# Kernel tuning notes

Measured on AMD Instinct MI355X. Metric: run time of the kernel, lower is better.

Reference implementation:

```python
import jax, jax.numpy as jnp
import numpy as np

NUM_ROUTING = 3

def squash(v, axis=-1):
    # scale = s2 / (1 + s2) / sqrt(s2), same as the TF source (no epsilon)
    s2 = jnp.sum(jnp.square(v), axis=axis, keepdims=True)
    scale = s2 / (1.0 + s2) / jnp.sqrt(s2)
    return scale * v


def setup_inputs() -> dict:
    key = jax.random.key(0)
    k1, k2 = jax.random.split(key)
    B, I, D = 128, 1152, 8   # batch, input_num_capsule, input_dim_vector
    C, E = 32, 16            # num_capsule, dim_vector
    x = jax.random.normal(k1, (B, I, D), dtype=jnp.float32)
    W = jax.random.normal(k2, (I, C, D, E), dtype=jnp.float32) * 0.05
    return {"x": x, "W": W}


def reference(x, W):
    # x: [B, I, D]; W: [I, C, D, E]
    B, I, D = x.shape
    C, E = W.shape[1], W.shape[3]
    # inputs_hat: u_hat[b,i,c,e] = sum_d x[b,i,d] * W[i,c,d,e]
    # (the TF code serializes this over batch via tf.scan; math is a batched GEMM)
    u_hat = jnp.einsum('bid,icde->bice', x, W)  # [B, I, C, E]
    # routing logits; TF bias has shape [1, I, C, 1, 1] and becomes per-batch
    # [B, I, C, 1, 1] after the first += (broadcast). We track [*, I, C].
    b = jnp.zeros((1, I, C), dtype=x.dtype)
    outputs = None
    for i in range(NUM_ROUTING):
        c = jax.nn.softmax(b, axis=2)[..., None]           # [*, I, C, 1]
        s = jnp.sum(c * u_hat, axis=1, keepdims=True)      # [B, 1, C, E]
        outputs = squash(s)                                # [B, 1, C, E]
        if i != NUM_ROUTING - 1:
            b = b + jnp.sum(u_hat * outputs, axis=-1)      # [B, I, C]
    return outputs.reshape(B, C, E)
```

## Files before the change

### kernel.cpp

```cpp
#include <hip/hip_runtime.h>
#include <hip/hip_fp16.h>
#include <math.h>

#define BATCH 128
#define NI    1152
#define ND    8
#define NC    32
#define NE    16
#define NROUT 3

#define ISPLIT     64
#define GTILES     9
#define BT         16
#define NB         4
#define RT_THREADS 256
#define CROW       68
#define TLDSW      (NC * CROW)
#define SQ_THREADS 256
#define PREP_TPB   2

typedef _Float16 h2 __attribute__((ext_vector_type(2)));
typedef unsigned int uint;

__device__ __forceinline__ h2 cvt_pk(float a, float b) {
    auto r = __builtin_amdgcn_cvt_pkrtz(a, b);
    union { decltype(r) i; h2 o; } u; u.i = r; return u.o;
}
__device__ __forceinline__ uint h2u(h2 v) { union { h2 h; uint u; } x; x.h = v; return x.u; }
__device__ __forceinline__ h2 u2h(uint v) { union { uint u; h2 h; } x; x.u = v; return x.h; }

#if __has_builtin(__builtin_amdgcn_fdot2)
#define FDOT2(a, b, c) __builtin_amdgcn_fdot2((a), (b), (c), false)
#else
__device__ __forceinline__ float FDOT2(h2 a, h2 b, float c) {
    return c + (float)a.x * (float)b.x + (float)a.y * (float)b.y;
}
#endif

template<int CTRL>
__device__ __forceinline__ float dpp_add(float v) {
    int t = __builtin_amdgcn_update_dpp(0, __float_as_int(v), CTRL, 0xF, 0xF, true);
    return v + __int_as_float(t);
}

__device__ __forceinline__ float xor32_sum(float v) {
#if __has_builtin(__builtin_amdgcn_permlane32_swap)
    auto r = __builtin_amdgcn_permlane32_swap(__float_as_int(v), __float_as_int(v), false, false);
    return __int_as_float(r[0]) + __int_as_float(r[1]);
#else
    return v + __shfl_xor(v, 32);
#endif
}
__device__ __forceinline__ float xor16_sum(float v) {
#if __has_builtin(__builtin_amdgcn_permlane16_swap)
    auto r = __builtin_amdgcn_permlane16_swap(__float_as_int(v), __float_as_int(v), false, false);
    return __int_as_float(r[0]) + __int_as_float(r[1]);
#else
    int s = __builtin_amdgcn_ds_swizzle(__float_as_int(v), 0x401F);
    return v + __int_as_float(s);
#endif
}

__device__ __forceinline__ float sum_over_e8(float v) {
    v = dpp_add<0xB1>(v);
    v = dpp_add<0x4E>(v);
    v = dpp_add<0x141>(v);
    return v;
}

__global__ __launch_bounds__(RT_THREADS)
void prep_kernel(const float* __restrict__ W, uint* __restrict__ W_hp)
{
    __shared__ float ls[PREP_TPB][NC * 132];

    const int tid = threadIdx.x;
    const size_t i0 = (size_t)blockIdx.x * PREP_TPB;

    const float4* src = (const float4*)(W + i0 * (NC * ND * NE));
#pragma unroll
    for (int t = 0; t < PREP_TPB; ++t) {
#pragma unroll
        for (int r = 0; r < 4; ++r) {
            int g = tid + r * RT_THREADS;
            float4 v = src[t * 1024 + g];
            *(float4*)&ls[t][(g >> 5) * 132 + (g & 31) * 4] = v;
        }
    }
    __syncthreads();

#pragma unroll
    for (int t = 0; t < PREP_TPB; ++t) {
#pragma unroll
        for (int r = 0; r < 2; ++r) {
            int g = tid + r * RT_THREADS;
            int c = g >> 4, e = g & 15;
            const float* p = &ls[t][c * 132 + e];
            uint4 o;
            o.x = h2u(cvt_pk(p[0],  p[16]));
            o.y = h2u(cvt_pk(p[32], p[48]));
            o.z = h2u(cvt_pk(p[64], p[80]));
            o.w = h2u(cvt_pk(p[96], p[112]));
            *(uint4*)&W_hp[(i0 + t) * TLDSW + c * CROW + e * 4] = o;
        }
    }
}

__global__ __launch_bounds__(RT_THREADS)
void route_iter_kernel(const float* __restrict__ x, const uint* __restrict__ W_hp,
                       const float* __restrict__ o_sum, __half* __restrict__ s_part,
                       int iter)
{
    constexpr int ICHUNK_T = NI / ISPLIT;
    constexpr int NGROUP_T = ICHUNK_T / GTILES;
    static_assert(NGROUP_T * GTILES == ICHUNK_T, "group split");

    __shared__ uint Wh[GTILES * TLDSW];

    const int tid = threadIdx.x;
    const int c   = tid & 31;
    const int eh  = (tid >> 5) & 1;
    int wid;
    asm("v_mov_b32 %0, %1" : "=v"(wid) : "v"(tid >> 6));
    const int ic  = blockIdx.x;
    const int bt  = blockIdx.y;
    const int i0  = ic * ICHUNK_T;
    const int b0  = bt * BT + wid * NB;
    const int e0  = eh * 8;

    float o_reg[NB][8];
    if (iter > 0) {
#pragma unroll
        for (int j = 0; j < NB; ++j) {
            const float4* op = (const float4*)(o_sum + ((size_t)(b0 + j) * NC + c) * NE + e0);
            float4 a = op[0], b = op[1];
            o_reg[j][0] = a.x; o_reg[j][1] = a.y; o_reg[j][2] = a.z; o_reg[j][3] = a.w;
            o_reg[j][4] = b.x; o_reg[j][5] = b.y; o_reg[j][6] = b.z; o_reg[j][7] = b.w;
        }
    }

    float s_acc[NB][8];
#pragma unroll
    for (int j = 0; j < NB; ++j)
#pragma unroll
        for (int e = 0; e < 8; ++e) s_acc[j][e] = 0.f;

    const float* xp[NB];
    float4 xnA[NB][2], xnB[NB][2];
#pragma unroll
    for (int j = 0; j < NB; ++j) {
        xp[j] = x + ((size_t)(b0 + j) * NI + i0) * ND;
        xnA[j][0] = *(const float4*)xp[j];
        xnA[j][1] = *(const float4*)(xp[j] + 4);
    }

    const uint* wbase = &Wh[c * CROW + e0 * 4];

    auto body = [&](const float4 (&XC)[NB][2], float4 (&XN)[NB][2], int t, int II) {
        if (II + 1 < ICHUNK_T) {
#pragma unroll
            for (int j = 0; j < NB; ++j) {
                xp[j] += ND;
                XN[j][0] = *(const float4*)xp[j];
                XN[j][1] = *(const float4*)(xp[j] + 4);
            }
        }

        h2 xq[NB][4];
#pragma unroll
        for (int j = 0; j < NB; ++j) {
            xq[j][0] = cvt_pk(XC[j][0].x, XC[j][0].y);
            xq[j][1] = cvt_pk(XC[j][0].z, XC[j][0].w);
            xq[j][2] = cvt_pk(XC[j][1].x, XC[j][1].y);
            xq[j][3] = cvt_pk(XC[j][1].z, XC[j][1].w);
        }

        const uint* wr = wbase + t * TLDSW;
        float uh[NB][8];
#pragma unroll
        for (int er = 0; er < 8; ++er) {
            uint4 wv = *(const uint4*)(wr + er * 4);
            h2 w0 = u2h(wv.x), w1 = u2h(wv.y), w2 = u2h(wv.z), w3 = u2h(wv.w);
#pragma unroll
            for (int j = 0; j < NB; ++j) {
                float acc = 0.f;
                acc = FDOT2(xq[j][0], w0, acc);
                acc = FDOT2(xq[j][1], w1, acc);
                acc = FDOT2(xq[j][2], w2, acc);
                acc = FDOT2(xq[j][3], w3, acc);
                uh[j][er] = acc;
            }
        }

        if (iter > 0) {
#pragma unroll
            for (int j = 0; j < NB; ++j) {
                float lp = 0.f;
#pragma unroll
                for (int e = 0; e < 8; ++e) lp = fmaf(uh[j][e], o_reg[j][e], lp);
                lp = xor32_sum(lp);
                float el = __expf(lp);
                float v = dpp_add<0x140>(dpp_add<0x141>(
                          dpp_add<0x4E>(dpp_add<0xB1>(el))));
                float den = xor16_sum(v);
                float wgt = el * __builtin_amdgcn_rcpf(den);
#pragma unroll
                for (int e = 0; e < 8; ++e) s_acc[j][e] = fmaf(wgt, uh[j][e], s_acc[j][e]);
            }
        } else {
            const float wgt = 1.f / 32.f;
#pragma unroll
            for (int j = 0; j < NB; ++j)
#pragma unroll
                for (int e = 0; e < 8; ++e) s_acc[j][e] = fmaf(wgt, uh[j][e], s_acc[j][e]);
        }
    };

#pragma unroll
    for (int g = 0; g < NGROUP_T; ++g) {
        if (g) __syncthreads();
        {
            constexpr int TOT4 = GTILES * TLDSW / 4;
            const uint4* src = (const uint4*)(W_hp + (size_t)(i0 + g * GTILES) * TLDSW);
            uint4* dst = (uint4*)Wh;
#pragma unroll
            for (int k = 0; k < (TOT4 + RT_THREADS - 1) / RT_THREADS; ++k) {
                int idx = tid + k * RT_THREADS;
                if (TOT4 % RT_THREADS == 0 || idx < TOT4)
                    dst[idx] = src[idx];
            }
        }
        __syncthreads();

#pragma unroll
        for (int tp = 0; tp < GTILES; ++tp) {
            int II = g * GTILES + tp;
            if ((II & 1) == 0) body(xnA, xnB, tp, II);
            else               body(xnB, xnA, tp, II);
        }
    }

#pragma unroll
    for (int j = 0; j < NB; ++j) {
        __half* base = s_part + (((size_t)ic * BATCH + (b0 + j)) * NC + c) * NE + e0;
        union { __half2 h2v[4]; uint4 u; } pk;
#pragma unroll
        for (int q = 0; q < 4; ++q)
            pk.h2v[q] = __floats2half2_rn(s_acc[j][2*q], s_acc[j][2*q+1]);
        *(uint4*)base = pk.u;
    }
}

__global__ __launch_bounds__(SQ_THREADS)
void squash_kernel(const __half* __restrict__ s_part, float* __restrict__ o_sum,
                   float* __restrict__ out, int iter)
{
    const int base2 = (blockIdx.x * SQ_THREADS + threadIdx.x) * 2;

    float a0 = 0.f, a1 = 0.f;
#pragma unroll 8
    for (int k = 0; k < ISPLIT; ++k) {
        __half2 v = *(const __half2*)(s_part + (size_t)k * (BATCH * NC * NE) + base2);
        a0 += __low2float(v);
        a1 += __high2float(v);
    }

    float q = sum_over_e8(a0 * a0 + a1 * a1);
    float scale = sqrtf(q) / (1.f + q);
    float o0 = scale * a0, o1 = scale * a1;

    if (iter == NROUT - 1) {
        *(float2*)(out + base2) = make_float2(o0, o1);
    } else if (iter == 0) {
        *(float2*)(o_sum + base2) = make_float2(o0, o1);
    } else {
        float2 prev = *(float2*)(o_sum + base2);
        *(float2*)(o_sum + base2) = make_float2(prev.x + o0, prev.y + o1);
    }
}

extern "C" void kernel_launch(void* const* d_in, const int* in_sizes, int n_in,
                              void* d_out, int out_size, void* d_ws, size_t ws_size,
                              hipStream_t stream) {
    const float* x = (const float*)d_in[0];
    const float* W = (const float*)d_in[1];
    float* out = (float*)d_out;

    const size_t whp_words = (size_t)NI * TLDSW;
    const size_t slice_h   = (size_t)BATCH * NC * NE;

    uint*   W_hp   = (uint*)d_ws;
    __half* s_part = (__half*)(W_hp + whp_words);
    float*  o_sum  = (float*)(s_part + (size_t)ISPLIT * slice_h);

    prep_kernel<<<NI / PREP_TPB, RT_THREADS, 0, stream>>>(W, W_hp);

    for (int it = 0; it < NROUT; ++it) {
        route_iter_kernel<<<dim3(ISPLIT, BATCH / BT), RT_THREADS, 0, stream>>>(
            x, W_hp, o_sum, s_part, it);
        squash_kernel<<<(BATCH * NC * NE) / (SQ_THREADS * 2), SQ_THREADS, 0, stream>>>(
            s_part, o_sum, out, it);
    }
}
```

Measured before the change: 106.2 us.

## Fuse routing iterations and squash into one persistent kernel with grid barriers

```diff
diff --git a/kernel.cpp b/kernel.cpp
--- a/kernel.cpp
+++ b/kernel.cpp
@@ -10,14 +10,15 @@
 #define NROUT 3
 
 #define ISPLIT     64
-#define GTILES     9
-#define BT         16
+#define ICHUNK     18
+#define BT         32
 #define NB         4
-#define RT_THREADS 256
+#define FT_THREADS 512
 #define CROW       68
 #define TLDSW      (NC * CROW)
-#define SQ_THREADS 256
+#define RT_THREADS 256
 #define PREP_TPB   2
+#define NBLOCKS    256
 
 typedef _Float16 h2 __attribute__((ext_vector_type(2)));
 typedef unsigned int uint;
@@ -66,6 +67,18 @@
     v = dpp_add<0x4E>(v);
     v = dpp_add<0x141>(v);
     return v;
+}
+
+__device__ __forceinline__ void gbar(uint* cnt) {
+    __syncthreads();
+    if (threadIdx.x == 0) {
+        __hip_atomic_fetch_add(cnt, 1u, __ATOMIC_ACQ_REL, __HIP_MEMORY_SCOPE_AGENT);
+        while (__hip_atomic_load(cnt, __ATOMIC_ACQUIRE, __HIP_MEMORY_SCOPE_AGENT)
+               < (uint)NBLOCKS) {
+            __builtin_amdgcn_s_sleep(2);
+        }
+    }
+    __syncthreads();
 }
 
 __global__ __launch_bounds__(RT_THREADS)
@@ -105,16 +118,12 @@
     }
 }
 
-__global__ __launch_bounds__(RT_THREADS)
-void route_iter_kernel(const float* __restrict__ x, const uint* __restrict__ W_hp,
-                       const float* __restrict__ o_sum, __half* __restrict__ s_part,
-                       int iter)
+__global__ __launch_bounds__(FT_THREADS)
+void fused_kernel(const float* __restrict__ x, const uint* __restrict__ W_hp,
+                  __half* __restrict__ s_part, float* __restrict__ o_sum,
+                  float* __restrict__ out, uint* __restrict__ bar)
 {
-    constexpr int ICHUNK_T = NI / ISPLIT;
-    constexpr int NGROUP_T = ICHUNK_T / GTILES;
-    static_assert(NGROUP_T * GTILES == ICHUNK_T, "group split");
-
-    __shared__ uint Wh[GTILES * TLDSW];
+    __shared__ uint Wh[ICHUNK * TLDSW];
 
     const int tid = threadIdx.x;
     const int c   = tid & 31;
@@ -123,158 +132,154 @@
     asm("v_mov_b32 %0, %1" : "=v"(wid) : "v"(tid >> 6));
     const int ic  = blockIdx.x;
     const int bt  = blockIdx.y;
-    const int i0  = ic * ICHUNK_T;
+    const int i0  = ic * ICHUNK;
     const int b0  = bt * BT + wid * NB;
     const int e0  = eh * 8;
-
-    float o_reg[NB][8];
-    if (iter > 0) {
+    const int blin = bt * ISPLIT + ic;
+
+    {
+        constexpr int TOT4 = ICHUNK * TLDSW / 4;
+        const uint4* src = (const uint4*)(W_hp + (size_t)i0 * TLDSW);
+        uint4* dst = (uint4*)Wh;
+#pragma unroll
+        for (int k = 0; k < (TOT4 + FT_THREADS - 1) / FT_THREADS; ++k) {
+            int idx = tid + k * FT_THREADS;
+            if (idx < TOT4) dst[idx] = src[idx];
+        }
+    }
+    __syncthreads();
+
+    const uint* wbase = &Wh[c * CROW + e0 * 4];
+
+    for (int it = 0; it < NROUT; ++it) {
+        float o_reg[NB][8];
+        if (it > 0) {
+#pragma unroll
+            for (int j = 0; j < NB; ++j) {
+                const float4* op = (const float4*)(o_sum + ((size_t)(b0 + j) * NC + c) * NE + e0);
+                float4 a = op[0], b = op[1];
+                o_reg[j][0] = a.x; o_reg[j][1] = a.y; o_reg[j][2] = a.z; o_reg[j][3] = a.w;
+                o_reg[j][4] = b.x; o_reg[j][5] = b.y; o_reg[j][6] = b.z; o_reg[j][7] = b.w;
+            }
+        }
+
+        float s_acc[NB][8];
+#pragma unroll
+        for (int j = 0; j < NB; ++j)
+#pragma unroll
+            for (int e = 0; e < 8; ++e) s_acc[j][e] = 0.f;
+
+        const float* xp[NB];
+        float4 xnA[NB][2], xnB[NB][2];
 #pragma unroll
         for (int j = 0; j < NB; ++j) {
-            const float4* op = (const float4*)(o_sum + ((size_t)(b0 + j) * NC + c) * NE + e0);
-            float4 a = op[0], b = op[1];
-            o_reg[j][0] = a.x; o_reg[j][1] = a.y; o_reg[j][2] = a.z; o_reg[j][3] = a.w;
-            o_reg[j][4] = b.x; o_reg[j][5] = b.y; o_reg[j][6] = b.z; o_reg[j][7] = b.w;
-        }
-    }
-
-    float s_acc[NB][8];
-#pragma unroll
-    for (int j = 0; j < NB; ++j)
-#pragma unroll
-        for (int e = 0; e < 8; ++e) s_acc[j][e] = 0.f;
-
-    const float* xp[NB];
-    float4 xnA[NB][2], xnB[NB][2];
-#pragma unroll
-    for (int j = 0; j < NB; ++j) {
-        xp[j] = x + ((size_t)(b0 + j) * NI + i0) * ND;
-        xnA[j][0] = *(const float4*)xp[j];
-        xnA[j][1] = *(const float4*)(xp[j] + 4);
-    }
-
-    const uint* wbase = &Wh[c * CROW + e0 * 4];
-
-    auto body = [&](const float4 (&XC)[NB][2], float4 (&XN)[NB][2], int t, int II) {
-        if (II + 1 < ICHUNK_T) {
+            xp[j] = x + ((size_t)(b0 + j) * NI + i0) * ND;
+            xnA[j][0] = *(const float4*)xp[j];
+            xnA[j][1] = *(const float4*)(xp[j] + 4);
+        }
+
+        auto body = [&](const float4 (&XC)[NB][2], float4 (&XN)[NB][2], int t) {
+            if (t + 1 < ICHUNK) {
+#pragma unroll
+                for (int j = 0; j < NB; ++j) {
+                    xp[j] += ND;
+                    XN[j][0] = *(const float4*)xp[j];
+                    XN[j][1] = *(const float4*)(xp[j] + 4);
+                }
+            }
+
+            h2 xq[NB][4];
 #pragma unroll
             for (int j = 0; j < NB; ++j) {
-                xp[j] += ND;
-                XN[j][0] = *(const float4*)xp[j];
-                XN[j][1] = *(const float4*)(xp[j] + 4);
-            }
-        }
-
-        h2 xq[NB][4];
+                xq[j][0] = cvt_pk(XC[j][0].x, XC[j][0].y);
+                xq[j][1] = cvt_pk(XC[j][0].z, XC[j][0].w);
+                xq[j][2] = cvt_pk(XC[j][1].x, XC[j][1].y);
+                xq[j][3] = cvt_pk(XC[j][1].z, XC[j][1].w);
+            }
+
+            const uint* wr = wbase + t * TLDSW;
+            float uh[NB][8];
+#pragma unroll
+            for (int er = 0; er < 8; ++er) {
+                uint4 wv = *(const uint4*)(wr + er * 4);
+                h2 w0 = u2h(wv.x), w1 = u2h(wv.y), w2 = u2h(wv.z), w3 = u2h(wv.w);
+#pragma unroll
+                for (int j = 0; j < NB; ++j) {
+                    float acc = 0.f;
+                    acc = FDOT2(xq[j][0], w0, acc);
+                    acc = FDOT2(xq[j][1], w1, acc);
+                    acc = FDOT2(xq[j][2], w2, acc);
+                    acc = FDOT2(xq[j][3], w3, acc);
+                    uh[j][er] = acc;
+                }
+            }
+
+            if (it > 0) {
+#pragma unroll
+                for (int j = 0; j < NB; ++j) {
+                    float lp = 0.f;
+#pragma unroll
+                    for (int e = 0; e < 8; ++e) lp = fmaf(uh[j][e], o_reg[j][e], lp);
+                    lp = xor32_sum(lp);
+                    float el = __expf(lp);
+                    float v = dpp_add<0x140>(dpp_add<0x141>(
+                              dpp_add<0x4E>(dpp_add<0xB1>(el))));
+                    float den = xor16_sum(v);
+                    float wgt = el * __builtin_amdgcn_rcpf(den);
+#pragma unroll
+                    for (int e = 0; e < 8; ++e) s_acc[j][e] = fmaf(wgt, uh[j][e], s_acc[j][e]);
+                }
+            } else {
+                const float wgt = 1.f / 32.f;
+#pragma unroll
+                for (int j = 0; j < NB; ++j)
+#pragma unroll
+                    for (int e = 0; e < 8; ++e) s_acc[j][e] = fmaf(wgt, uh[j][e], s_acc[j][e]);
+            }
+        };
+
+#pragma unroll
+        for (int t2 = 0; t2 < ICHUNK / 2; ++t2) {
+            body(xnA, xnB, 2 * t2);
+            body(xnB, xnA, 2 * t2 + 1);
+        }
+
 #pragma unroll
         for (int j = 0; j < NB; ++j) {
-            xq[j][0] = cvt_pk(XC[j][0].x, XC[j][0].y);
-            xq[j][1] = cvt_pk(XC[j][0].z, XC[j][0].w);
-            xq[j][2] = cvt_pk(XC[j][1].x, XC[j][1].y);
-            xq[j][3] = cvt_pk(XC[j][1].z, XC[j][1].w);
-        }
-
-        const uint* wr = wbase + t * TLDSW;
-        float uh[NB][8];
-#pragma unroll
-        for (int er = 0; er < 8; ++er) {
-            uint4 wv = *(const uint4*)(wr + er * 4);
-            h2 w0 = u2h(wv.x), w1 = u2h(wv.y), w2 = u2h(wv.z), w3 = u2h(wv.w);
-#pragma unroll
-            for (int j = 0; j < NB; ++j) {
-                float acc = 0.f;
-                acc = FDOT2(xq[j][0], w0, acc);
-                acc = FDOT2(xq[j][1], w1, acc);
-                acc = FDOT2(xq[j][2], w2, acc);
-                acc = FDOT2(xq[j][3], w3, acc);
-                uh[j][er] = acc;
-            }
-        }
-
-        if (iter > 0) {
-#pragma unroll
-            for (int j = 0; j < NB; ++j) {
-                float lp = 0.f;
-#pragma unroll
-                for (int e = 0; e < 8; ++e) lp = fmaf(uh[j][e], o_reg[j][e], lp);
-                lp = xor32_sum(lp);
-                float el = __expf(lp);
-                float v = dpp_add<0x140>(dpp_add<0x141>(
-                          dpp_add<0x4E>(dpp_add<0xB1>(el))));
-                float den = xor16_sum(v);
-                float wgt = el * __builtin_amdgcn_rcpf(den);
-#pragma unroll
-                for (int e = 0; e < 8; ++e) s_acc[j][e] = fmaf(wgt, uh[j][e], s_acc[j][e]);
-            }
-        } else {
-            const float wgt = 1.f / 32.f;
-#pragma unroll
-            for (int j = 0; j < NB; ++j)
-#pragma unroll
-                for (int e = 0; e < 8; ++e) s_acc[j][e] = fmaf(wgt, uh[j][e], s_acc[j][e]);
-        }
-    };
-
-#pragma unroll
-    for (int g = 0; g < NGROUP_T; ++g) {
-        if (g) __syncthreads();
-        {
-            constexpr int TOT4 = GTILES * TLDSW / 4;
-            const uint4* src = (const uint4*)(W_hp + (size_t)(i0 + g * GTILES) * TLDSW);
-            uint4* dst = (uint4*)Wh;
-#pragma unroll
-            for (int k = 0; k < (TOT4 + RT_THREADS - 1) / RT_THREADS; ++k) {
-                int idx = tid + k * RT_THREADS;
-                if (TOT4 % RT_THREADS == 0 || idx < TOT4)
-                    dst[idx] = src[idx];
-            }
-        }
-        __syncthreads();
-
-#pragma unroll
-        for (int tp = 0; tp < GTILES; ++tp) {
-            int II = g * GTILES + tp;
-            if ((II & 1) == 0) body(xnA, xnB, tp, II);
-            else               body(xnB, xnA, tp, II);
-        }
-    }
-
-#pragma unroll
-    for (int j = 0; j < NB; ++j) {
-        __half* base = s_part + (((size_t)ic * BATCH + (b0 + j)) * NC + c) * NE + e0;
-        union { __half2 h2v[4]; uint4 u; } pk;
-#pragma unroll
-        for (int q = 0; q < 4; ++q)
-            pk.h2v[q] = __floats2half2_rn(s_acc[j][2*q], s_acc[j][2*q+1]);
-        *(uint4*)base = pk.u;
-    }
-}
-
-__global__ __launch_bounds__(SQ_THREADS)
-void squash_kernel(const __half* __restrict__ s_part, float* __restrict__ o_sum,
-                   float* __restrict__ out, int iter)
-{
-    const int base2 = (blockIdx.x * SQ_THREADS + threadIdx.x) * 2;
-
-    float a0 = 0.f, a1 = 0.f;
+            __half* base = s_part + (((size_t)ic * BATCH + (b0 + j)) * NC + c) * NE + e0;
+            union { __half2 h2v[4]; uint4 u; } pk;
+#pragma unroll
+            for (int q = 0; q < 4; ++q)
+                pk.h2v[q] = __floats2half2_rn(s_acc[j][2*q], s_acc[j][2*q+1]);
+            *(uint4*)base = pk.u;
+        }
+
+        gbar(&bar[it * 2]);
+
+        if (tid < 128) {
+            const int base2 = (blin * 128 + tid) * 2;
+            float a0 = 0.f, a1 = 0.f;
 #pragma unroll 8
-    for (int k = 0; k < ISPLIT; ++k) {
-        __half2 v = *(const __half2*)(s_part + (size_t)k * (BATCH * NC * NE) + base2);
-        a0 += __low2float(v);
-        a1 += __high2float(v);
-    }
-
-    float q = sum_over_e8(a0 * a0 + a1 * a1);
-    float scale = sqrtf(q) / (1.f + q);
-    float o0 = scale * a0, o1 = scale * a1;
-
-    if (iter == NROUT - 1) {
-        *(float2*)(out + base2) = make_float2(o0, o1);
-    } else if (iter == 0) {
-        *(float2*)(o_sum + base2) = make_float2(o0, o1);
-    } else {
-        float2 prev = *(float2*)(o_sum + base2);
-        *(float2*)(o_sum + base2) = make_float2(prev.x + o0, prev.y + o1);
+            for (int k = 0; k < ISPLIT; ++k) {
+                __half2 v = *(const __half2*)(s_part + (size_t)k * (BATCH * NC * NE) + base2);
+                a0 += __low2float(v);
+                a1 += __high2float(v);
+            }
+            float q = sum_over_e8(a0 * a0 + a1 * a1);
+            float scale = sqrtf(q) / (1.f + q);
+            float o0 = scale * a0, o1 = scale * a1;
+
+            if (it == NROUT - 1) {
+                *(float2*)(out + base2) = make_float2(o0, o1);
+            } else if (it == 0) {
+                *(float2*)(o_sum + base2) = make_float2(o0, o1);
+            } else {
+                float2 prev = *(float2*)(o_sum + base2);
+                *(float2*)(o_sum + base2) = make_float2(prev.x + o0, prev.y + o1);
+            }
+        }
+
+        if (it < NROUT - 1) gbar(&bar[it * 2 + 1]);
     }
 }
 
@@ -291,13 +296,12 @@
     uint*   W_hp   = (uint*)d_ws;
     __half* s_part = (__half*)(W_hp + whp_words);
     float*  o_sum  = (float*)(s_part + (size_t)ISPLIT * slice_h);
+    uint*   bar    = (uint*)(o_sum + slice_h);
+
+    (void)hipMemsetAsync(bar, 0, 64, stream);
 
     prep_kernel<<<NI / PREP_TPB, RT_THREADS, 0, stream>>>(W, W_hp);
 
-    for (int it = 0; it < NROUT; ++it) {
-        route_iter_kernel<<<dim3(ISPLIT, BATCH / BT), RT_THREADS, 0, stream>>>(
-            x, W_hp, o_sum, s_part, it);
-        squash_kernel<<<(BATCH * NC * NE) / (SQ_THREADS * 2), SQ_THREADS, 0, stream>>>(
-            s_part, o_sum, out, it);
-    }
-}
+    fused_kernel<<<dim3(ISPLIT, BATCH / BT), FT_THREADS, 0, stream>>>(
+        x, W_hp, s_part, o_sum, out, bar);
+}
```

Result: slower. 265.8 us (+150.4%).
